# Kernel tuning notes

Measured on AMD Instinct MI355X. Metric: run time of the kernel, lower is better.

Reference implementation:

```python
import jax, jax.numpy as jnp
import numpy as np

EPS = 1e-4      # geomloss: eps = blur**p = 0.01**2
N_ITERS = 20    # fixed Sinkhorn iterations
UNI_T = 2.0     # uniformity temperature (Wang & Isola)


def _sqdist(x, y):
    # [N,D],[M,D] -> [N,M] squared euclidean distances
    return jnp.sum((x[:, None, :] - y[None, :, :]) ** 2, axis=-1)


def _cost(x, y):
    # geomloss p=2 cost: ||x-y||^2 / 2
    return 0.5 * _sqdist(x, y)


def _softmin(C, h):
    # f_i = -eps * log( (1/M) * sum_j exp((h_j - C_ij)/eps) )
    M = C.shape[1]
    lse = jax.nn.logsumexp((h[None, :] - C) / EPS, axis=1)
    return -EPS * (lse - jnp.log(jnp.float32(M)))


def _sinkhorn_potentials(C):
    # alternating log-domain Sinkhorn updates, uniform weights
    def body(carry, _):
        f, g = carry
        f = _softmin(C, g)
        g = _softmin(C.T, f)
        return (f, g), None
    init = (jnp.zeros(C.shape[0], C.dtype), jnp.zeros(C.shape[1], C.dtype))
    (f, g), _ = jax.lax.scan(body, init, None, length=N_ITERS)
    return f, g


def _sym_potential(C):
    # symmetric fixed-point for the debiasing terms OT_eps(a,a)
    def body(p, _):
        return 0.5 * (p + _softmin(C, p)), None
    p, _ = jax.lax.scan(body, jnp.zeros(C.shape[0], C.dtype), None, length=N_ITERS)
    return p


def sinkhorn_divergence(x, y):
    # debiased: S = OT(x,y) - 0.5*OT(x,x) - 0.5*OT(y,y); envelope-theorem grads
    Cxy = _cost(x, y)
    f_d, g_d = _sinkhorn_potentials(jax.lax.stop_gradient(Cxy))
    f = _softmin(Cxy, jax.lax.stop_gradient(g_d))          # final differentiable step
    g = _softmin(Cxy.T, jax.lax.stop_gradient(f_d))

    Cxx = _cost(x, x)
    px = _sym_potential(jax.lax.stop_gradient(Cxx))
    fx = _softmin(Cxx, jax.lax.stop_gradient(px))          # 0.5*OT(x,x) = mean(fx)

    Cyy = _cost(y, y)
    py = _sym_potential(jax.lax.stop_gradient(Cyy))
    fy = _softmin(Cyy, jax.lax.stop_gradient(py))

    return jnp.mean(f) + jnp.mean(g) - jnp.mean(fx) - jnp.mean(fy)


def uniformity(x):
    # log E_{i != j} [ exp(-t * ||x_i - x_j||^2) ]
    N = x.shape[0]
    D = _sqdist(x, x)
    D = D + jnp.diag(jnp.full((N,), jnp.inf, dtype=x.dtype))  # mask self-pairs
    return jax.nn.logsumexp(-UNI_T * D) - jnp.log(jnp.float32(N * (N - 1)))


def setup_inputs() -> dict:
    key = jax.random.key(0)
    k1, k2 = jax.random.split(key)
    p_q = jax.random.normal(k1, (4096, 3), dtype=jnp.float32)
    p_gt = jax.random.normal(k2, (4096, 4), dtype=jnp.float32)
    return {"p_q": p_q, "p_gt": p_gt}


def reference(p_q, p_gt):
    L = sinkhorn_divergence(p_q, p_gt[:, :3])
    L = L + uniformity(p_q)
    return L
```

## Files before the change

### kernel.cpp

```cpp
#include <hip/hip_runtime.h>

#define NPT  4096
#define NBLK 256
#define NTHR 1024

constexpr float EPSV   = 1e-4f;
constexpr float LN2F   = 0.69314718055994531f;
constexpr float E2     = EPSV * LN2F;
constexpr float INV_E2 = 1.0f / E2;
constexpr float S_U    = 4.0f / LN2F;

#define SMEM_FLOATS 33024
#define SMEM_BYTES  (SMEM_FLOATS * 4)

__device__ __forceinline__ float fexp2(float x) { return __builtin_amdgcn_exp2f(x); }
__device__ __forceinline__ float flog2(float x) { return __builtin_amdgcn_logf(x); }

__device__ __forceinline__ float gload(const float* p) {
    return __hip_atomic_load(p, __ATOMIC_RELAXED, __HIP_MEMORY_SCOPE_SYSTEM);
}
__device__ __forceinline__ void gstore(float* p, float v) {
    __hip_atomic_store(p, v, __ATOMIC_RELAXED, __HIP_MEMORY_SCOPE_SYSTEM);
}

__device__ __forceinline__ void group_barrier(unsigned* base, unsigned target, int b) {
    asm volatile("s_waitcnt vmcnt(0)" ::: "memory");
    __syncthreads();
    if (threadIdx.x == 0) {
        __hip_atomic_fetch_add(&base[(b & 15) * 16], 1u,
                               __ATOMIC_RELAXED, __HIP_MEMORY_SCOPE_SYSTEM);
        for (;;) {
            unsigned tot = 0;
#pragma unroll
            for (int i = 0; i < 16; ++i)
                tot += __hip_atomic_load(&base[i * 16],
                                         __ATOMIC_RELAXED, __HIP_MEMORY_SCOPE_SYSTEM);
            if (tot >= target) break;
            __builtin_amdgcn_s_sleep(1);
        }
    }
    __syncthreads();
}

template<bool ISU>
__device__ __forceinline__ void run_task(
    const float4* __restrict__ cp,
    const float4* __restrict__ rp,
    int r0g, int half, int lane, float scale, float2* part, int lr0)
{
    float xs0[2], xs1[2], xs2[2];
#pragma unroll
    for (int r = 0; r < 2; ++r) {
        float4 q = rp[r0g + r];
        xs0[r] = q.x * scale; xs1[r] = q.y * scale; xs2[r] = q.z * scale;
    }
    const float4* col = cp + half * 2048 + lane;
    float m[2], s[2];

#pragma unroll
    for (int chunk = 0; chunk < 2; ++chunk) {
        float av[2][16];
        float mc[2] = {-1e30f, -1e30f};
#pragma unroll
        for (int k = 0; k < 16; ++k) {
            const float4 c = col[chunk * 1024 + k * 64];
#pragma unroll
            for (int r = 0; r < 2; ++r) {
                float a = fmaf(xs0[r], c.x, c.w);
                a = fmaf(xs1[r], c.y, a);
                a = fmaf(xs2[r], c.z, a);
                if (ISU) {
                    const int j = half * 2048 + chunk * 1024 + k * 64 + lane;
                    a = (j == r0g + r) ? -1e30f : a;
                }
                av[r][k] = a;
                mc[r] = fmaxf(mc[r], a);
            }
        }
#pragma unroll
        for (int r = 0; r < 2; ++r) {
            float sc_ = 0.0f;
#pragma unroll
            for (int k = 0; k < 16; ++k) sc_ += fexp2(av[r][k] - mc[r]);
            if (chunk == 0) { m[r] = mc[r]; s[r] = sc_; }
            else {
                float d = m[r] - mc[r];
                float e = fexp2(-fabsf(d));
                float bigs   = (d >= 0.0f) ? s[r] : sc_;
                float smalls = (d >= 0.0f) ? sc_  : s[r];
                s[r] = fmaf(smalls, e, bigs);
                m[r] = fmaxf(m[r], mc[r]);
            }
        }
    }
    float ml[2] = {m[0], m[1]};
#pragma unroll
    for (int off = 1; off < 64; off <<= 1) {
#pragma unroll
        for (int r = 0; r < 2; ++r)
            m[r] = fmaxf(m[r], __shfl_xor(m[r], off, 64));
    }
#pragma unroll
    for (int r = 0; r < 2; ++r) s[r] *= fexp2(ml[r] - m[r]);
#pragma unroll
    for (int off = 1; off < 64; off <<= 1) {
#pragma unroll
        for (int r = 0; r < 2; ++r)
            s[r] += __shfl_xor(s[r], off, 64);
    }
    if (lane == 0) {
        part[(lr0 + 0) * 2 + half] = make_float2(m[0], s[0]);
        part[(lr0 + 1) * 2 + half] = make_float2(m[1], s[1]);
    }
}

__global__ void sink_init(float* __restrict__ ws) {
    int t = blockIdx.x * blockDim.x + threadIdx.x;
    if (t < NPT) {
        gstore(ws + t, 0.0f);
        gstore(ws + 4096 + t, 0.0f);
        gstore(ws + 8192 + t, 0.0f);
        gstore(ws + 16384 + t, 0.0f);
    }
    if (t < 512) {
        __hip_atomic_store((unsigned*)(ws + 40960) + t, 0u,
                           __ATOMIC_RELAXED, __HIP_MEMORY_SCOPE_SYSTEM);
    }
}

__global__ __launch_bounds__(NTHR)
__attribute__((amdgpu_waves_per_eu(4, 4)))
void sink_main(
    const float* __restrict__ xin, const float* __restrict__ yin,
    float* __restrict__ ws, float* __restrict__ out)
{
    extern __shared__ float smem[];
    float4* packx = (float4*)smem;
    float4* packy = (float4*)(smem + 16384);
    float2* part  = (float2*)(smem + 32768);

    float* f    = ws;
    float* g    = ws + 4096;
    float* px0  = ws + 8192;
    float* px1  = ws + 12288;
    float* py0  = ws + 16384;
    float* py1  = ws + 20480;
    float* ffin = ws + 24576;
    float* fxv  = ws + 28672;
    float* fyv  = ws + 32768;
    float* uls  = ws + 36864;
    unsigned* ctrA = (unsigned*)(ws + 40960);
    unsigned* ctrB = (unsigned*)(ws + 40960) + 256;

    const int tid  = threadIdx.x;
    const int b    = blockIdx.x;
    const int wave = tid >> 6;
    const int lane = tid & 63;
    unsigned* cbarrier = (b < 128) ? ctrA : ctrB;

    for (int i = tid; i < NPT; i += NTHR) {
        packx[i] = make_float4(xin[3 * i], xin[3 * i + 1], xin[3 * i + 2], 0.0f);
        float4 v = ((const float4*)yin)[i];
        packy[i] = make_float4(v.x, v.y, v.z, 0.0f);
    }
    __syncthreads();

    for (int h = 0; h <= 40; ++h) {
        bool rows_x, cols_x, isU = false, avg = false;
        const float* pot; float* outp; float scale = INV_E2;
        int row0g, rows_pb;
        if (h == 0) {
            if (b < 128)      { rows_x = true;  cols_x = false; pot = g;    outp = f;    rows_pb = 32; row0g = b * 32; }
            else if (b < 192) { rows_x = true;  cols_x = true;  pot = px0;  outp = px1;  avg = true; rows_pb = 64; row0g = (b - 128) * 64; }
            else              { rows_x = true;  cols_x = true;  pot = nullptr; outp = uls; isU = true; scale = S_U; rows_pb = 64; row0g = (b - 192) * 64; }
        } else if (h == 40) {
            if (b < 128)      { rows_x = true;  cols_x = false; pot = g;    outp = ffin; rows_pb = 32; row0g = b * 32; }
            else if (b < 192) { rows_x = true;  cols_x = true;  pot = px0;  outp = fxv;  rows_pb = 64; row0g = (b - 128) * 64; }
            else              { rows_x = false; cols_x = false; pot = py0;  outp = fyv;  rows_pb = 64; row0g = (b - 192) * 64; }
        } else if (h & 1) {
            int k = (h - 1) >> 1;
            if (b < 128) { rows_x = false; cols_x = true;  pot = f; outp = g; rows_pb = 32; row0g = b * 32; }
            else         { rows_x = false; cols_x = false; pot = (k & 1) ? py1 : py0; outp = (k & 1) ? py0 : py1; avg = true; rows_pb = 32; row0g = (b - 128) * 32; }
        } else {
            int k = h >> 1;
            if (b < 128) { rows_x = true; cols_x = false; pot = g; outp = f; rows_pb = 32; row0g = b * 32; }
            else         { rows_x = true; cols_x = true;  pot = (k & 1) ? px1 : px0; outp = (k & 1) ? px0 : px1; avg = true; rows_pb = 32; row0g = (b - 128) * 32; }
        }

        float4* colpk = cols_x ? packx : packy;
        for (int j = tid; j < NPT; j += NTHR) {
            float4 c = colpk[j];
            float cn = 0.5f * (c.x * c.x + c.y * c.y) + 0.5f * c.z * c.z;
            float pv = pot ? gload(pot + j) : 0.0f;
            colpk[j].w = (pv - cn) * scale;
        }
        __syncthreads();

        const float4* rowpk = rows_x ? packx : packy;
        const int ntask = rows_pb;
        for (int t = wave; t < ntask; t += 16) {
            int grp = t >> 1, half = t & 1;
            int lr0 = grp << 1;
            int r0g = row0g + lr0;
            if (isU) run_task<true >(colpk, rowpk, r0g, half, lane, scale, part, lr0);
            else     run_task<false>(colpk, rowpk, r0g, half, lane, scale, part, lr0);
        }
        __syncthreads();

        if (tid < rows_pb) {
            float2 pa = part[tid * 2 + 0], pb = part[tid * 2 + 1];
            float mm = fmaxf(pa.x, pb.x);
            float ss = pa.y * fexp2(pa.x - mm) + pb.y * fexp2(pb.x - mm);
            int rg = row0g + tid;
            float4 q = rowpk[rg];
            float rn = 0.5f * (q.x * q.x + q.y * q.y) + 0.5f * q.z * q.z;
            float lse2 = mm + flog2(ss) - rn * scale;
            float val;
            if (isU) {
                val = lse2;
            } else {
                val = -E2 * (lse2 - 12.0f);
                if (avg) val = 0.5f * (gload(pot + rg) + val);
            }
            gstore(outp + rg, val);
        }

        group_barrier(cbarrier, 128u * (unsigned)(h + 1), b);
    }

    if (b == 0) {
        if (tid == 0) {
            for (;;) {
                unsigned tot = 0;
#pragma unroll
                for (int i = 0; i < 16; ++i)
                    tot += __hip_atomic_load(&ctrB[i * 16],
                                             __ATOMIC_RELAXED, __HIP_MEMORY_SCOPE_SYSTEM);
                if (tot >= 128u * 41u) break;
                __builtin_amdgcn_s_sleep(1);
            }
        }
        __syncthreads();

        float sf = 0.f, sg = 0.f, sx = 0.f, sy = 0.f, um = -1e30f, us = 0.f;
        for (int i = tid; i < NPT; i += NTHR) {
            sf += gload(ffin + i); sg += gload(g + i);
            sx += gload(fxv + i);  sy += gload(fyv + i);
            float v = gload(uls + i);
            float mn = fmaxf(um, v);
            us = us * fexp2(um - mn) + fexp2(v - mn);
            um = mn;
        }
#pragma unroll
        for (int off = 1; off < 64; off <<= 1) {
            sf += __shfl_xor(sf, off, 64);
            sg += __shfl_xor(sg, off, 64);
            sx += __shfl_xor(sx, off, 64);
            sy += __shfl_xor(sy, off, 64);
            float mo = __shfl_xor(um, off, 64);
            float so = __shfl_xor(us, off, 64);
            float mn = fmaxf(um, mo);
            us = us * fexp2(um - mn) + so * fexp2(mo - mn);
            um = mn;
        }
        __syncthreads();
        if (lane == 0) {
            float* red = smem;
            red[wave * 6 + 0] = sf; red[wave * 6 + 1] = sg; red[wave * 6 + 2] = sx;
            red[wave * 6 + 3] = sy; red[wave * 6 + 4] = um; red[wave * 6 + 5] = us;
        }
        __syncthreads();
        if (tid == 0) {
            float* red = smem;
            float Sf = 0, Sg = 0, Sx = 0, Sy = 0, Um = -1e30f, Us = 0;
            for (int w = 0; w < 16; ++w) {
                Sf += red[w * 6 + 0]; Sg += red[w * 6 + 1];
                Sx += red[w * 6 + 2]; Sy += red[w * 6 + 3];
                float mo = red[w * 6 + 4], so = red[w * 6 + 5];
                float mn = fmaxf(Um, mo);
                Us = Us * fexp2(Um - mn) + so * fexp2(mo - mn);
                Um = mn;
            }
            float mean = (Sf + Sg - Sx - Sy) * (1.0f / 4096.0f);
            float U = LN2F * (Um + flog2(Us)) - logf(4096.0f * 4095.0f);
            out[0] = mean + U;
        }
    }
}

extern "C" void kernel_launch(void* const* d_in, const int* in_sizes, int n_in,
                              void* d_out, int out_size, void* d_ws, size_t ws_size,
                              hipStream_t stream) {
    const float* x = (const float*)d_in[0];
    const float* y = (const float*)d_in[1];
    float* ws  = (float*)d_ws;
    float* out = (float*)d_out;

    (void)hipFuncSetAttribute((const void*)sink_main,
                              hipFuncAttributeMaxDynamicSharedMemorySize, SMEM_BYTES);

    sink_init<<<4, 1024, 0, stream>>>(ws);
    sink_main<<<NBLK, NTHR, SMEM_BYTES, stream>>>(x, y, ws, out);
}
```

Before: 538.9 us.

## Pair columns in SoA-packed LDS layout and compute with packed FP32 FMA

Changes the shared-memory point layout from one float4 per point to two float4 arrays holding coordinate pairs for two adjacent points, so v_pk_fma_f32 can compute two cost-plus-potential values per instruction. The inner max uses v_max3_f32 and the exponent offsets use v_pk_add_f32. The aim is fewer VALU instructions in the dominant logsumexp loop. The cost is more complex indexing for rows and masking, and the exp2 count stays the same, so the gain is limited to the FMA/max part.

```diff
diff --git a/kernel.cpp b/kernel.cpp
--- a/kernel.cpp
+++ b/kernel.cpp
@@ -13,8 +13,26 @@
 #define SMEM_FLOATS 33024
 #define SMEM_BYTES  (SMEM_FLOATS * 4)
 
+typedef float v2f __attribute__((ext_vector_type(2)));
+
 __device__ __forceinline__ float fexp2(float x) { return __builtin_amdgcn_exp2f(x); }
 __device__ __forceinline__ float flog2(float x) { return __builtin_amdgcn_logf(x); }
+
+__device__ __forceinline__ v2f pk_fma(v2f a, v2f b, v2f c) {
+    v2f d;
+    asm("v_pk_fma_f32 %0, %1, %2, %3" : "=v"(d) : "v"(a), "v"(b), "v"(c));
+    return d;
+}
+__device__ __forceinline__ v2f pk_add(v2f a, v2f b) {
+    v2f d;
+    asm("v_pk_add_f32 %0, %1, %2" : "=v"(d) : "v"(a), "v"(b));
+    return d;
+}
+__device__ __forceinline__ float max3f(float a, float b, float c) {
+    float d;
+    asm("v_max3_f32 %0, %1, %2, %3" : "=v"(d) : "v"(a), "v"(b), "v"(c));
+    return d;
+}
 
 __device__ __forceinline__ float gload(const float* p) {
     return __hip_atomic_load(p, __ATOMIC_RELAXED, __HIP_MEMORY_SCOPE_SYSTEM);
@@ -44,50 +62,73 @@
 
 template<bool ISU>
 __device__ __forceinline__ void run_task(
-    const float4* __restrict__ cp,
-    const float4* __restrict__ rp,
+    const float4* __restrict__ cpA, const float4* __restrict__ cpB,
+    const float*  __restrict__ rAf, const float*  __restrict__ rBf,
     int r0g, int half, int lane, float scale, float2* part, int lr0)
 {
-    float xs0[2], xs1[2], xs2[2];
+    v2f xs0[2], xs1[2], xs2[2];
 #pragma unroll
     for (int r = 0; r < 2; ++r) {
-        float4 q = rp[r0g + r];
-        xs0[r] = q.x * scale; xs1[r] = q.y * scale; xs2[r] = q.z * scale;
-    }
-    const float4* col = cp + half * 2048 + lane;
+        const int rr = r0g + r;
+        const int pb4 = (rr >> 1) * 4, c0 = rr & 1;
+        float xv = rAf[pb4 + c0] * scale;
+        float yv = rAf[pb4 + 2 + c0] * scale;
+        float zv = rBf[pb4 + c0] * scale;
+        xs0[r].x = xv; xs0[r].y = xv;
+        xs1[r].x = yv; xs1[r].y = yv;
+        xs2[r].x = zv; xs2[r].y = zv;
+    }
     float m[2], s[2];
-
-#pragma unroll
-    for (int chunk = 0; chunk < 2; ++chunk) {
-        float av[2][16];
+    const int pbase = half * 1024 + lane;
+    const float4* colA = cpA + pbase;
+    const float4* colB = cpB + pbase;
+
+#pragma unroll
+    for (int chunk = 0; chunk < 4; ++chunk) {
+        v2f av[2][4];
         float mc[2] = {-1e30f, -1e30f};
 #pragma unroll
-        for (int k = 0; k < 16; ++k) {
-            const float4 c = col[chunk * 1024 + k * 64];
+        for (int k = 0; k < 4; ++k) {
+            const float4 a4 = colA[(chunk * 4 + k) * 64];
+            const float4 b4 = colB[(chunk * 4 + k) * 64];
+            v2f xx; xx.x = a4.x; xx.y = a4.y;
+            v2f yy; yy.x = a4.z; yy.y = a4.w;
+            v2f zz; zz.x = b4.x; zz.y = b4.y;
+            v2f gg; gg.x = b4.z; gg.y = b4.w;
 #pragma unroll
             for (int r = 0; r < 2; ++r) {
-                float a = fmaf(xs0[r], c.x, c.w);
-                a = fmaf(xs1[r], c.y, a);
-                a = fmaf(xs2[r], c.z, a);
+                v2f a01 = pk_fma(xs2[r], zz, gg);
+                a01 = pk_fma(xs1[r], yy, a01);
+                a01 = pk_fma(xs0[r], xx, a01);
                 if (ISU) {
-                    const int j = half * 2048 + chunk * 1024 + k * 64 + lane;
-                    a = (j == r0g + r) ? -1e30f : a;
+                    const int p = pbase + (chunk * 4 + k) * 64;
+                    const int rr = r0g + r;
+                    if (p == (rr >> 1)) {
+                        if (rr & 1) a01.y = -1e30f; else a01.x = -1e30f;
+                    }
                 }
-                av[r][k] = a;
-                mc[r] = fmaxf(mc[r], a);
+                av[r][k] = a01;
+                mc[r] = max3f(mc[r], a01.x, a01.y);
             }
         }
 #pragma unroll
         for (int r = 0; r < 2; ++r) {
-            float sc_ = 0.0f;
-#pragma unroll
-            for (int k = 0; k < 16; ++k) sc_ += fexp2(av[r][k] - mc[r]);
+            const float nm = -mc[r];
+            v2f mcn; mcn.x = nm; mcn.y = nm;
+            float sA = 0.0f, sB = 0.0f;
+#pragma unroll
+            for (int k = 0; k < 4; ++k) {
+                v2f d = pk_add(av[r][k], mcn);
+                sA += fexp2(d.x);
+                sB += fexp2(d.y);
+            }
+            const float sc_ = sA + sB;
             if (chunk == 0) { m[r] = mc[r]; s[r] = sc_; }
             else {
-                float d = m[r] - mc[r];
-                float e = fexp2(-fabsf(d));
-                float bigs   = (d >= 0.0f) ? s[r] : sc_;
-                float smalls = (d >= 0.0f) ? sc_  : s[r];
+                float dd = m[r] - mc[r];
+                float e = fexp2(-fabsf(dd));
+                float bigs   = (dd >= 0.0f) ? s[r] : sc_;
+                float smalls = (dd >= 0.0f) ? sc_  : s[r];
                 s[r] = fmaf(smalls, e, bigs);
                 m[r] = fmaxf(m[r], mc[r]);
             }
@@ -135,9 +176,11 @@
     float* __restrict__ ws, float* __restrict__ out)
 {
     extern __shared__ float smem[];
-    float4* packx = (float4*)smem;
-    float4* packy = (float4*)(smem + 16384);
-    float2* part  = (float2*)(smem + 32768);
+    float4* pAx = (float4*)smem;
+    float4* pBx = (float4*)(smem + 8192);
+    float4* pAy = (float4*)(smem + 16384);
+    float4* pBy = (float4*)(smem + 24576);
+    float2* part = (float2*)(smem + 32768);
 
     float* f    = ws;
     float* g    = ws + 4096;
@@ -158,10 +201,15 @@
     const int lane = tid & 63;
     unsigned* cbarrier = (b < 128) ? ctrA : ctrB;
 
-    for (int i = tid; i < NPT; i += NTHR) {
-        packx[i] = make_float4(xin[3 * i], xin[3 * i + 1], xin[3 * i + 2], 0.0f);
-        float4 v = ((const float4*)yin)[i];
-        packy[i] = make_float4(v.x, v.y, v.z, 0.0f);
+    const float4* yin4 = (const float4*)yin;
+    for (int i = tid; i < 2048; i += NTHR) {
+        float x0 = xin[6 * i + 0], y0v = xin[6 * i + 1], z0 = xin[6 * i + 2];
+        float x1 = xin[6 * i + 3], y1v = xin[6 * i + 4], z1 = xin[6 * i + 5];
+        pAx[i] = make_float4(x0, x1, y0v, y1v);
+        pBx[i] = make_float4(z0, z1, 0.0f, 0.0f);
+        float4 v0 = yin4[2 * i], v1 = yin4[2 * i + 1];
+        pAy[i] = make_float4(v0.x, v1.x, v0.y, v1.y);
+        pBy[i] = make_float4(v0.z, v1.z, 0.0f, 0.0f);
     }
     __syncthreads();
 
@@ -187,23 +235,29 @@
             else         { rows_x = true; cols_x = true;  pot = (k & 1) ? px1 : px0; outp = (k & 1) ? px0 : px1; avg = true; rows_pb = 32; row0g = (b - 128) * 32; }
         }
 
-        float4* colpk = cols_x ? packx : packy;
-        for (int j = tid; j < NPT; j += NTHR) {
-            float4 c = colpk[j];
-            float cn = 0.5f * (c.x * c.x + c.y * c.y) + 0.5f * c.z * c.z;
-            float pv = pot ? gload(pot + j) : 0.0f;
-            colpk[j].w = (pv - cn) * scale;
-        }
-        __syncthreads();
-
-        const float4* rowpk = rows_x ? packx : packy;
+        float4* cpA = cols_x ? pAx : pAy;
+        float4* cpB = cols_x ? pBx : pBy;
+        for (int p = tid; p < 2048; p += NTHR) {
+            float4 a4 = cpA[p];
+            float4 b4 = cpB[p];
+            float cn0 = 0.5f * (a4.x * a4.x + a4.z * a4.z + b4.x * b4.x);
+            float cn1 = 0.5f * (a4.y * a4.y + a4.w * a4.w + b4.y * b4.y);
+            float pv0 = pot ? gload(pot + 2 * p)     : 0.0f;
+            float pv1 = pot ? gload(pot + 2 * p + 1) : 0.0f;
+            ((float2*)&cpB[p])[1] = make_float2((pv0 - cn0) * scale,
+                                                (pv1 - cn1) * scale);
+        }
+        __syncthreads();
+
+        const float* rAf = (const float*)(rows_x ? pAx : pAy);
+        const float* rBf = (const float*)(rows_x ? pBx : pBy);
         const int ntask = rows_pb;
         for (int t = wave; t < ntask; t += 16) {
             int grp = t >> 1, half = t & 1;
             int lr0 = grp << 1;
             int r0g = row0g + lr0;
-            if (isU) run_task<true >(colpk, rowpk, r0g, half, lane, scale, part, lr0);
-            else     run_task<false>(colpk, rowpk, r0g, half, lane, scale, part, lr0);
+            if (isU) run_task<true >(cpA, cpB, rAf, rBf, r0g, half, lane, scale, part, lr0);
+            else     run_task<false>(cpA, cpB, rAf, rBf, r0g, half, lane, scale, part, lr0);
         }
         __syncthreads();
 
@@ -212,8 +266,11 @@
             float mm = fmaxf(pa.x, pb.x);
             float ss = pa.y * fexp2(pa.x - mm) + pb.y * fexp2(pb.x - mm);
             int rg = row0g + tid;
-            float4 q = rowpk[rg];
-            float rn = 0.5f * (q.x * q.x + q.y * q.y) + 0.5f * q.z * q.z;
+            const int pb4 = (rg >> 1) * 4, c0 = rg & 1;
+            float xv = rAf[pb4 + c0];
+            float yv = rAf[pb4 + 2 + c0];
+            float zv = rBf[pb4 + c0];
+            float rn = 0.5f * (xv * xv + yv * yv + zv * zv);
             float lse2 = mm + flog2(ss) - rn * scale;
             float val;
             if (isU) {
```

Measured after the change: 535.3 us. About the same (-0.7%).

## Block four rows per wave, use DPP partial reductions, precompute point norms

Applied to the files above, without the earlier changes.

Each wave now handles four rows per task instead of two, so every column float4 read from LDS feeds twice as many FMAs. The column sweep is split into eight chunks of four columns, which keeps register pressure manageable. The full 64-lane shuffle reduction is replaced by three DPP steps that reduce within groups of eight lanes. This leaves sixteen partial (max, sum) pairs per row for the final combine. Squared norms are computed once in the init kernel and read from the workspace, instead of being recomputed from the packed points in every half-iteration. The trade-off is more LDS partial traffic and more work in the final per-row combine.

```diff
diff --git a/kernel.cpp b/kernel.cpp
--- a/kernel.cpp
+++ b/kernel.cpp
@@ -10,11 +10,37 @@
 constexpr float INV_E2 = 1.0f / E2;
 constexpr float S_U    = 4.0f / LN2F;
 
-#define SMEM_FLOATS 33024
+#define SMEM_FLOATS 34816
 #define SMEM_BYTES  (SMEM_FLOATS * 4)
+
+#define WF    0
+#define WG    4096
+#define WPX0  8192
+#define WPX1  12288
+#define WPY0  16384
+#define WPY1  20480
+#define WFFIN 24576
+#define WFXV  28672
+#define WFYV  32768
+#define WULS  36864
+#define WCTR  40960
+#define WCNX  41984
+#define WCNY  46080
 
 __device__ __forceinline__ float fexp2(float x) { return __builtin_amdgcn_exp2f(x); }
 __device__ __forceinline__ float flog2(float x) { return __builtin_amdgcn_logf(x); }
+
+__device__ __forceinline__ float max3f(float a, float b, float c) {
+    float d;
+    asm("v_max3_f32 %0, %1, %2, %3" : "=v"(d) : "v"(a), "v"(b), "v"(c));
+    return d;
+}
+
+template<int CTRL>
+__device__ __forceinline__ float dppf(float x) {
+    return __int_as_float(__builtin_amdgcn_update_dpp(
+        __float_as_int(x), __float_as_int(x), CTRL, 0xF, 0xF, false));
+}
 
 __device__ __forceinline__ float gload(const float* p) {
     return __hip_atomic_load(p, __ATOMIC_RELAXED, __HIP_MEMORY_SCOPE_SYSTEM);
@@ -44,86 +70,85 @@
 
 template<bool ISU>
 __device__ __forceinline__ void run_task(
-    const float4* __restrict__ cp,
-    const float4* __restrict__ rp,
-    int r0g, int half, int lane, float scale, float2* part, int lr0)
+    const float4* __restrict__ colpk, const float4* __restrict__ rowpk,
+    int r0g, int half, int lane, float scale, float2* part2, int lr0)
 {
-    float xs0[2], xs1[2], xs2[2];
-#pragma unroll
-    for (int r = 0; r < 2; ++r) {
-        float4 q = rp[r0g + r];
+    float xs0[4], xs1[4], xs2[4];
+#pragma unroll
+    for (int r = 0; r < 4; ++r) {
+        float4 q = rowpk[r0g + r];
         xs0[r] = q.x * scale; xs1[r] = q.y * scale; xs2[r] = q.z * scale;
     }
-    const float4* col = cp + half * 2048 + lane;
-    float m[2], s[2];
-
-#pragma unroll
-    for (int chunk = 0; chunk < 2; ++chunk) {
-        float av[2][16];
-        float mc[2] = {-1e30f, -1e30f};
-#pragma unroll
-        for (int k = 0; k < 16; ++k) {
-            const float4 c = col[chunk * 1024 + k * 64];
-#pragma unroll
-            for (int r = 0; r < 2; ++r) {
+    float m[4], s[4];
+    const int cbase = half * 2048 + lane;
+    const float4* col = colpk + cbase;
+
+#pragma unroll
+    for (int chunk = 0; chunk < 8; ++chunk) {
+        float av[4][4];
+        float mc[4] = {-1e30f, -1e30f, -1e30f, -1e30f};
+#pragma unroll
+        for (int k = 0; k < 4; ++k) {
+            const float4 c = col[(chunk * 4 + k) * 64];
+#pragma unroll
+            for (int r = 0; r < 4; ++r) {
                 float a = fmaf(xs0[r], c.x, c.w);
                 a = fmaf(xs1[r], c.y, a);
                 a = fmaf(xs2[r], c.z, a);
                 if (ISU) {
-                    const int j = half * 2048 + chunk * 1024 + k * 64 + lane;
-                    a = (j == r0g + r) ? -1e30f : a;
+                    const int j = cbase + (chunk * 4 + k) * 64;
+                    if (j == r0g + r) a = -1e30f;
                 }
                 av[r][k] = a;
                 mc[r] = fmaxf(mc[r], a);
             }
         }
 #pragma unroll
-        for (int r = 0; r < 2; ++r) {
-            float sc_ = 0.0f;
-#pragma unroll
-            for (int k = 0; k < 16; ++k) sc_ += fexp2(av[r][k] - mc[r]);
+        for (int r = 0; r < 4; ++r) {
+            float sc_ = fexp2(av[r][0] - mc[r]) + fexp2(av[r][1] - mc[r])
+                      + fexp2(av[r][2] - mc[r]) + fexp2(av[r][3] - mc[r]);
             if (chunk == 0) { m[r] = mc[r]; s[r] = sc_; }
             else {
-                float d = m[r] - mc[r];
-                float e = fexp2(-fabsf(d));
-                float bigs   = (d >= 0.0f) ? s[r] : sc_;
-                float smalls = (d >= 0.0f) ? sc_  : s[r];
+                float dd = m[r] - mc[r];
+                float e = fexp2(-fabsf(dd));
+                float bigs   = (dd >= 0.0f) ? s[r] : sc_;
+                float smalls = (dd >= 0.0f) ? sc_  : s[r];
                 s[r] = fmaf(smalls, e, bigs);
                 m[r] = fmaxf(m[r], mc[r]);
             }
         }
     }
-    float ml[2] = {m[0], m[1]};
-#pragma unroll
-    for (int off = 1; off < 64; off <<= 1) {
-#pragma unroll
-        for (int r = 0; r < 2; ++r)
-            m[r] = fmaxf(m[r], __shfl_xor(m[r], off, 64));
-    }
-#pragma unroll
-    for (int r = 0; r < 2; ++r) s[r] *= fexp2(ml[r] - m[r]);
-#pragma unroll
-    for (int off = 1; off < 64; off <<= 1) {
-#pragma unroll
-        for (int r = 0; r < 2; ++r)
-            s[r] += __shfl_xor(s[r], off, 64);
-    }
-    if (lane == 0) {
-        part[(lr0 + 0) * 2 + half] = make_float2(m[0], s[0]);
-        part[(lr0 + 1) * 2 + half] = make_float2(m[1], s[1]);
-    }
-}
-
-__global__ void sink_init(float* __restrict__ ws) {
+#pragma unroll
+    for (int r = 0; r < 4; ++r) {
+        const float ml = m[r];
+        float mm = m[r];
+        mm = fmaxf(mm, dppf<0xB1>(mm));
+        mm = fmaxf(mm, dppf<0x4E>(mm));
+        mm = fmaxf(mm, dppf<0x141>(mm));
+        float ssv = s[r] * fexp2(ml - mm);
+        ssv += dppf<0xB1>(ssv);
+        ssv += dppf<0x4E>(ssv);
+        ssv += dppf<0x141>(ssv);
+        if ((lane & 7) == 0)
+            part2[(lr0 + r) * 16 + half * 8 + (lane >> 3)] = make_float2(mm, ssv);
+    }
+}
+
+__global__ void sink_init(const float* __restrict__ xin, const float* __restrict__ yin,
+                          float* __restrict__ ws) {
     int t = blockIdx.x * blockDim.x + threadIdx.x;
     if (t < NPT) {
-        gstore(ws + t, 0.0f);
-        gstore(ws + 4096 + t, 0.0f);
-        gstore(ws + 8192 + t, 0.0f);
-        gstore(ws + 16384 + t, 0.0f);
+        gstore(ws + WF + t, 0.0f);
+        gstore(ws + WG + t, 0.0f);
+        gstore(ws + WPX0 + t, 0.0f);
+        gstore(ws + WPY0 + t, 0.0f);
+        float x0 = xin[3 * t], y0 = xin[3 * t + 1], z0 = xin[3 * t + 2];
+        ws[WCNX + t] = 0.5f * (x0 * x0 + y0 * y0 + z0 * z0);
+        float4 v = ((const float4*)yin)[t];
+        ws[WCNY + t] = 0.5f * (v.x * v.x + v.y * v.y + v.z * v.z);
     }
     if (t < 512) {
-        __hip_atomic_store((unsigned*)(ws + 40960) + t, 0u,
+        __hip_atomic_store((unsigned*)(ws + WCTR) + t, 0u,
                            __ATOMIC_RELAXED, __HIP_MEMORY_SCOPE_SYSTEM);
     }
 }
@@ -137,20 +162,22 @@
     extern __shared__ float smem[];
     float4* packx = (float4*)smem;
     float4* packy = (float4*)(smem + 16384);
-    float2* part  = (float2*)(smem + 32768);
-
-    float* f    = ws;
-    float* g    = ws + 4096;
-    float* px0  = ws + 8192;
-    float* px1  = ws + 12288;
-    float* py0  = ws + 16384;
-    float* py1  = ws + 20480;
-    float* ffin = ws + 24576;
-    float* fxv  = ws + 28672;
-    float* fyv  = ws + 32768;
-    float* uls  = ws + 36864;
-    unsigned* ctrA = (unsigned*)(ws + 40960);
-    unsigned* ctrB = (unsigned*)(ws + 40960) + 256;
+    float2* part2 = (float2*)(smem + 32768);
+
+    float* f    = ws + WF;
+    float* g    = ws + WG;
+    float* px0  = ws + WPX0;
+    float* px1  = ws + WPX1;
+    float* py0  = ws + WPY0;
+    float* py1  = ws + WPY1;
+    float* ffin = ws + WFFIN;
+    float* fxv  = ws + WFXV;
+    float* fyv  = ws + WFYV;
+    float* uls  = ws + WULS;
+    unsigned* ctrA = (unsigned*)(ws + WCTR);
+    unsigned* ctrB = (unsigned*)(ws + WCTR) + 256;
+    const float* cnx = ws + WCNX;
+    const float* cny = ws + WCNY;
 
     const int tid  = threadIdx.x;
     const int b    = blockIdx.x;
@@ -188,32 +215,39 @@
         }
 
         float4* colpk = cols_x ? packx : packy;
+        const float* ccn = cols_x ? cnx : cny;
         for (int j = tid; j < NPT; j += NTHR) {
-            float4 c = colpk[j];
-            float cn = 0.5f * (c.x * c.x + c.y * c.y) + 0.5f * c.z * c.z;
             float pv = pot ? gload(pot + j) : 0.0f;
-            colpk[j].w = (pv - cn) * scale;
+            float cn = ccn[j];
+            ((float*)&colpk[j])[3] = (pv - cn) * scale;
         }
         __syncthreads();
 
         const float4* rowpk = rows_x ? packx : packy;
-        const int ntask = rows_pb;
+        const int ntask = rows_pb >> 1;
         for (int t = wave; t < ntask; t += 16) {
             int grp = t >> 1, half = t & 1;
-            int lr0 = grp << 1;
+            int lr0 = grp << 2;
             int r0g = row0g + lr0;
-            if (isU) run_task<true >(colpk, rowpk, r0g, half, lane, scale, part, lr0);
-            else     run_task<false>(colpk, rowpk, r0g, half, lane, scale, part, lr0);
-        }
-        __syncthreads();
-
+            if (isU) run_task<true >(colpk, rowpk, r0g, half, lane, scale, part2, lr0);
+            else     run_task<false>(colpk, rowpk, r0g, half, lane, scale, part2, lr0);
+        }
+        __syncthreads();
+
+        const float* rcn = rows_x ? cnx : cny;
         if (tid < rows_pb) {
-            float2 pa = part[tid * 2 + 0], pb = part[tid * 2 + 1];
-            float mm = fmaxf(pa.x, pb.x);
-            float ss = pa.y * fexp2(pa.x - mm) + pb.y * fexp2(pb.x - mm);
+            float2 pv2[16];
+#pragma unroll
+            for (int q = 0; q < 16; ++q) pv2[q] = part2[tid * 16 + q];
+            float mm = pv2[0].x;
+#pragma unroll
+            for (int q = 1; q < 15; q += 2) mm = max3f(mm, pv2[q].x, pv2[q + 1].x);
+            mm = fmaxf(mm, pv2[15].x);
+            float ss = 0.0f;
+#pragma unroll
+            for (int q = 0; q < 16; ++q) ss += pv2[q].y * fexp2(pv2[q].x - mm);
             int rg = row0g + tid;
-            float4 q = rowpk[rg];
-            float rn = 0.5f * (q.x * q.x + q.y * q.y) + 0.5f * q.z * q.z;
+            float rn = rcn[rg];
             float lse2 = mm + flog2(ss) - rn * scale;
             float val;
             if (isU) {
@@ -299,6 +333,6 @@
     (void)hipFuncSetAttribute((const void*)sink_main,
                               hipFuncAttributeMaxDynamicSharedMemorySize, SMEM_BYTES);
 
-    sink_init<<<4, 1024, 0, stream>>>(ws);
+    sink_init<<<4, 1024, 0, stream>>>(x, y, ws);
     sink_main<<<NBLK, NTHR, SMEM_BYTES, stream>>>(x, y, ws, out);
 }
```

Result: slower. 993.7 us (+84.4%).
